# Kernel tuning notes

Measured on AMD Instinct MI355X. Metric: run time of the kernel, lower is better.

Reference implementation:

```python
import jax, jax.numpy as jnp
from jax import lax
import numpy as np

MEM_SZ = 1024
SOMA_FAST = 4.0
SOMA_SLOW = 7.0
MOD_BIAS = 0.4
EPS_BASE = 0.9
BIAS_MOD_RANGE = 5.0


def setup_inputs() -> dict:
    key = jax.random.key(0)
    k1, k2, k3 = jax.random.split(key, 3)
    B, L, IN = 128, 512, 512
    u = jax.random.normal(k1, (B, L, IN), dtype=jnp.float32)
    h0 = jnp.zeros((2, B, MEM_SZ), dtype=jnp.float32)
    W_im = jax.random.normal(k2, (2 * MEM_SZ, IN), dtype=jnp.float32) * 0.05
    b_im = jax.random.normal(k3, (2 * MEM_SZ,), dtype=jnp.float32) * 0.05
    return {"u": u, "h0": h0, "W_im": W_im, "b_im": b_im}


def reference(u, h0, W_im, b_im):
    # Hoisted input projection: one big GEMM over all timesteps.
    # in_emb: [B, L, 2*mem]
    in_emb = jnp.einsum('bli,oi->blo', u, W_im) + b_im
    c1 = in_emb[..., :MEM_SZ]          # soma_bias_contribution_1
    i_o = in_emb[..., MEM_SZ:]
    soma_bias = jnp.tanh(c1 / BIAS_MOD_RANGE) * BIAS_MOD_RANGE

    def step(carry, inp):
        hf, hs = carry
        sb, io = inp
        hfn = jnp.tanh(io + SOMA_FAST * hf
                       - SOMA_SLOW * jnp.square(hs + MOD_BIAS) + sb)
        # variable_eps: 0.9 + 0.9 / (1 + exp((hf - 0.5) / -0.1))
        eps = EPS_BASE + EPS_BASE * jax.nn.sigmoid((hf - 0.5) * 10.0)
        hsn = (1.0 - eps) * hs + eps * hf
        return (hfn, hsn), hfn

    # scan over time: inputs as [L, B, mem]
    xs = (jnp.transpose(soma_bias, (1, 0, 2)), jnp.transpose(i_o, (1, 0, 2)))
    (hf_last, _hs_last), hf_seq = lax.scan(step, (h0[0], h0[1]), xs)
    h_t = jnp.transpose(hf_seq, (1, 0, 2))  # [B, L, mem]
    return h_t, hf_last
```

## Files before the change

kernel.cpp:

```cpp
#include <hip/hip_runtime.h>
#include <hip/hip_fp16.h>

#define MEM  1024
#define B_   128
#define L_   512
#define M_   (B_*L_)
#define N_   (2*MEM)
#define K_   512

#define SCALE_U 16.0f
#define SCALE_W 1024.0f
#define INV_SCALE (1.0f / (16.0f * 1024.0f))

typedef __attribute__((ext_vector_type(8))) _Float16 half8;
typedef __attribute__((ext_vector_type(4))) float f32x4;

__device__ __forceinline__ float fast_tanh(float x) {
    float e = __expf(2.0f * x);
    return 1.0f - 2.0f / (e + 1.0f);
}
__device__ __forceinline__ float fast_sigmoid(float x) {
    return 1.0f / (1.0f + __expf(-x));
}
__device__ __forceinline__ void gl_lds16(const void* g, void* l) {
    __builtin_amdgcn_global_load_lds(
        (const __attribute__((address_space(1))) void*)g,
        (__attribute__((address_space(3))) void*)l, 16, 0, 0);
}

__global__ void split_fp32_fp16x2(const float* __restrict__ in,
                                  unsigned short* __restrict__ hi,
                                  unsigned short* __restrict__ lo,
                                  int n4, float scale) {
    int i = blockIdx.x * 256 + threadIdx.x;
    if (i >= n4) return;
    const float4 v = reinterpret_cast<const float4*>(in)[i];
    float vs[4] = {v.x, v.y, v.z, v.w};
    unsigned short hs_[4], ls_[4];
#pragma unroll
    for (int c = 0; c < 4; ++c) {
        float xs = vs[c] * scale;
        __half h = __float2half_rn(xs);
        float r = xs - __half2float(h);
        __half l = __float2half_rn(r);
        hs_[c] = __half_as_ushort(h);
        ls_[c] = __half_as_ushort(l);
    }
    ushort4 h4, l4;
    h4.x = hs_[0]; h4.y = hs_[1]; h4.z = hs_[2]; h4.w = hs_[3];
    l4.x = ls_[0]; l4.y = ls_[1]; l4.z = ls_[2]; l4.w = ls_[3];
    reinterpret_cast<ushort4*>(hi)[i] = h4;
    reinterpret_cast<ushort4*>(lo)[i] = l4;
}

#define TM 128
#define TN 128
#define BK 32
__global__ __launch_bounds__(256, 2) void gemm_paired_kernel(
    const float* __restrict__ u,
    const unsigned short* __restrict__ wh, const unsigned short* __restrict__ wl,
    const float* __restrict__ bias,
    float* __restrict__ z_out) {
    __shared__ __attribute__((aligned(16))) float Af[TM * BK];
    __shared__ __attribute__((aligned(16))) unsigned short Bh0[TN * BK];
    __shared__ __attribute__((aligned(16))) unsigned short Bl0[TN * BK];
    __shared__ __attribute__((aligned(16))) unsigned short Bh1[TN * BK];
    __shared__ __attribute__((aligned(16))) unsigned short Bl1[TN * BK];

    const int tid = threadIdx.x;
    const int id  = blockIdx.x;
    const int mt  = (id >> 6) * 8 + (id & 7);
    const int nt  = (id >> 3) & 7;
    const int tileM = mt * TM;
    const int tileN = nt * TN;

    const int lane = tid & 63, w = tid >> 6;
    const int wm = w & 1, wn = w >> 1;
    const int lrow = lane & 15, quad = lane >> 4;
    const int q2 = quad ^ ((lrow >> 1) & 3);

    f32x4 acc0[4][4] = {};
    f32x4 acc1[4][4] = {};

    size_t aoff[4];
#pragma unroll
    for (int c = 0; c < 4; ++c) {
        const int p = c * 256 + tid;
        const int row = p >> 3;
        const int chunk = (p & 7) ^ (row & 7);
        aoff[c] = (size_t)(tileM + row) * K_ + chunk * 4;
    }
    const int i0 = tid, i1 = tid + 256;
    const int r0 = i0 >> 2, gs0 = (i0 & 3) ^ ((r0 >> 1) & 3);
    const int r1 = i1 >> 2, gs1 = (i1 & 3) ^ ((r1 >> 1) & 3);
    const size_t sB0a = (size_t)(tileN + r0) * K_ + gs0 * 8;
    const size_t sB0b = (size_t)(tileN + r1) * K_ + gs1 * 8;
    const size_t sB1a = (size_t)(tileN + 1024 + r0) * K_ + gs0 * 8;
    const size_t sB1b = (size_t)(tileN + 1024 + r1) * K_ + gs1 * 8;

    for (int kt = 0; kt < K_ / BK; ++kt) {
        const size_t ko = (size_t)kt * BK;
        __syncthreads();
#pragma unroll
        for (int c = 0; c < 4; ++c)
            gl_lds16(u + aoff[c] + ko, &Af[c * 1024 + tid * 4]);
        gl_lds16(wh + sB0a + ko, &Bh0[i0 * 8]);
        gl_lds16(wh + sB0b + ko, &Bh0[i1 * 8]);
        gl_lds16(wl + sB0a + ko, &Bl0[i0 * 8]);
        gl_lds16(wl + sB0b + ko, &Bl0[i1 * 8]);
        gl_lds16(wh + sB1a + ko, &Bh1[i0 * 8]);
        gl_lds16(wh + sB1b + ko, &Bh1[i1 * 8]);
        gl_lds16(wl + sB1a + ko, &Bl1[i0 * 8]);
        gl_lds16(wl + sB1b + ko, &Bl1[i1 * 8]);
        __syncthreads();

        half8 ahf[4], alf[4];
#pragma unroll
        for (int i = 0; i < 4; ++i) {
            const int r = wm * 64 + i * 16 + lrow;
            const int sw = r & 7;
            const f32x4 t0 = *(const f32x4*)&Af[(r * 8 + ((quad * 2)     ^ sw)) * 4];
            const f32x4 t1 = *(const f32x4*)&Af[(r * 8 + ((quad * 2 + 1) ^ sw)) * 4];
            half8 h, l;
#pragma unroll
            for (int e = 0; e < 4; ++e) {
                float xs = t0[e] * SCALE_U;
                _Float16 hh = (_Float16)xs;
                h[e] = hh;
                l[e] = (_Float16)(xs - (float)hh);
                xs = t1[e] * SCALE_U;
                hh = (_Float16)xs;
                h[e + 4] = hh;
                l[e + 4] = (_Float16)(xs - (float)hh);
            }
            ahf[i] = h; alf[i] = l;
        }
#pragma unroll
        for (int j = 0; j < 4; ++j) {
            const int bo = ((wn * 64 + j * 16 + lrow) * 4 + q2) * 8;
            const half8 b0h = *(const half8*)&Bh0[bo];
            const half8 b0l = *(const half8*)&Bl0[bo];
            const half8 b1h = *(const half8*)&Bh1[bo];
            const half8 b1l = *(const half8*)&Bl1[bo];
#pragma unroll
            for (int i = 0; i < 4; ++i) {
                f32x4 c0 = acc0[i][j];
                c0 = __builtin_amdgcn_mfma_f32_16x16x32_f16(ahf[i], b0h, c0, 0, 0, 0);
                c0 = __builtin_amdgcn_mfma_f32_16x16x32_f16(ahf[i], b0l, c0, 0, 0, 0);
                c0 = __builtin_amdgcn_mfma_f32_16x16x32_f16(alf[i], b0h, c0, 0, 0, 0);
                acc0[i][j] = c0;
                f32x4 c1 = acc1[i][j];
                c1 = __builtin_amdgcn_mfma_f32_16x16x32_f16(ahf[i], b1h, c1, 0, 0, 0);
                c1 = __builtin_amdgcn_mfma_f32_16x16x32_f16(ahf[i], b1l, c1, 0, 0, 0);
                c1 = __builtin_amdgcn_mfma_f32_16x16x32_f16(alf[i], b1h, c1, 0, 0, 0);
                acc1[i][j] = c1;
            }
        }
    }

#pragma unroll
    for (int j = 0; j < 4; ++j) {
        const int c = tileN + wn * 64 + j * 16 + lrow;
        const float b1v = bias[c];
        const float b2v = bias[c + 1024];
#pragma unroll
        for (int i = 0; i < 4; ++i) {
            const int rowb = tileM + wm * 64 + i * 16 + quad * 4;
#pragma unroll
            for (int r = 0; r < 4; ++r) {
                float v1 = acc0[i][j][r] * INV_SCALE + b1v;
                v1 = fast_tanh(v1 * 0.2f) * 5.0f;
                const float v2 = acc1[i][j][r] * INV_SCALE + b2v;
                z_out[(size_t)(rowb + r) * MEM + c] = v1 + v2;
            }
        }
    }
}

__global__ __launch_bounds__(256) void scan_kernel(
    const float* __restrict__ z,
    float* __restrict__ h_t,
    const float* __restrict__ h0,
    float* __restrict__ hf_last) {
    const int idx = blockIdx.x * 256 + threadIdx.x;
    const int b = idx >> 10, m = idx & (MEM - 1);
    float hf = h0[idx];
    float hs = h0[B_ * MEM + idx];
    const size_t base = (size_t)b * L_ * MEM + m;

    float zv[16], zn[16];
#pragma unroll
    for (int j = 0; j < 16; ++j) zv[j] = z[base + (size_t)j * MEM];

    for (int l0 = 0; l0 < L_; l0 += 16) {
        const bool more = (l0 + 16) < L_;
        if (more) {
#pragma unroll
            for (int j = 0; j < 16; ++j)
                zn[j] = z[base + (size_t)(l0 + 16 + j) * MEM];
        }
#pragma unroll
        for (int j = 0; j < 16; ++j) {
            const float hsb = hs + 0.4f;
            const float x = zv[j] + 4.0f * hf - 7.0f * hsb * hsb;
            const float hfn = fast_tanh(x);
            const float eps = 0.9f + 0.9f * fast_sigmoid(10.0f * (hf - 0.5f));
            hs = hs + eps * (hf - hs);
            h_t[base + (size_t)(l0 + j) * MEM] = hfn;
            hf = hfn;
        }
        if (more) {
#pragma unroll
            for (int j = 0; j < 16; ++j) zv[j] = zn[j];
        }
    }
    hf_last[idx] = hf;
}

extern "C" void kernel_launch(void* const* d_in, const int* in_sizes, int n_in,
                              void* d_out, int out_size, void* d_ws, size_t ws_size,
                              hipStream_t stream) {
    const float* u    = (const float*)d_in[0];
    const float* h0   = (const float*)d_in[1];
    const float* W_im = (const float*)d_in[2];
    const float* b_im = (const float*)d_in[3];

    float* out = (float*)d_out;
    float* h_t = out;
    float* hf_last = out + (size_t)M_ * MEM;

    char* ws = (char*)d_ws;
    float* z           = (float*)ws;
    unsigned short* wh = (unsigned short*)(ws + 268435456ull);
    unsigned short* wl = (unsigned short*)(ws + 270532608ull);

    {
        const int n4_w = (N_ * K_) / 4;
        split_fp32_fp16x2<<<(n4_w + 255) / 256, 256, 0, stream>>>(W_im, wh, wl, n4_w, SCALE_W);
    }
    {
        gemm_paired_kernel<<<4096, 256, 0, stream>>>(u, wh, wl, b_im, z);
    }
    {
        scan_kernel<<<(B_ * MEM) / 256, 256, 0, stream>>>(z, h_t, h0, hf_last);
    }
}
```

Before: 770.4 us.

## Double-buffer GEMM LDS tiles and enlarge M tile to 256 with 512 threads

The paired-fp16 GEMM now uses two LDS buffers. Global-to-LDS loads for the next K slice are issued before computing on the current one, which overlaps memory latency with MFMA work and removes one barrier per K step. The M tile doubles to 256 rows with 8 waves per block, halving the grid, and the MFMA section is wrapped in s_setprio to favour matrix issue. LDS per block grows to about 128KB, so only one block fits per CU, which may reduce latency hiding across blocks.

```diff
diff --git a/kernel.cpp b/kernel.cpp
--- a/kernel.cpp
+++ b/kernel.cpp
@@ -53,19 +53,19 @@
     reinterpret_cast<ushort4*>(lo)[i] = l4;
 }
 
-#define TM 128
+#define TM 256
 #define TN 128
 #define BK 32
-__global__ __launch_bounds__(256, 2) void gemm_paired_kernel(
+__global__ __launch_bounds__(512, 2) void gemm_paired_kernel(
     const float* __restrict__ u,
     const unsigned short* __restrict__ wh, const unsigned short* __restrict__ wl,
     const float* __restrict__ bias,
     float* __restrict__ z_out) {
-    __shared__ __attribute__((aligned(16))) float Af[TM * BK];
-    __shared__ __attribute__((aligned(16))) unsigned short Bh0[TN * BK];
-    __shared__ __attribute__((aligned(16))) unsigned short Bl0[TN * BK];
-    __shared__ __attribute__((aligned(16))) unsigned short Bh1[TN * BK];
-    __shared__ __attribute__((aligned(16))) unsigned short Bl1[TN * BK];
+    __shared__ __attribute__((aligned(16))) float Af[2][TM * BK];
+    __shared__ __attribute__((aligned(16))) unsigned short Bh0[2][TN * BK];
+    __shared__ __attribute__((aligned(16))) unsigned short Bl0[2][TN * BK];
+    __shared__ __attribute__((aligned(16))) unsigned short Bh1[2][TN * BK];
+    __shared__ __attribute__((aligned(16))) unsigned short Bl1[2][TN * BK];
 
     const int tid = threadIdx.x;
     const int id  = blockIdx.x;
@@ -75,7 +75,7 @@
     const int tileN = nt * TN;
 
     const int lane = tid & 63, w = tid >> 6;
-    const int wm = w & 1, wn = w >> 1;
+    const int wm = w & 3, wn = w >> 2;
     const int lrow = lane & 15, quad = lane >> 4;
     const int q2 = quad ^ ((lrow >> 1) & 3);
 
@@ -85,77 +85,88 @@
     size_t aoff[4];
 #pragma unroll
     for (int c = 0; c < 4; ++c) {
-        const int p = c * 256 + tid;
+        const int p = c * 512 + tid;
         const int row = p >> 3;
         const int chunk = (p & 7) ^ (row & 7);
         aoff[c] = (size_t)(tileM + row) * K_ + chunk * 4;
     }
-    const int i0 = tid, i1 = tid + 256;
-    const int r0 = i0 >> 2, gs0 = (i0 & 3) ^ ((r0 >> 1) & 3);
-    const int r1 = i1 >> 2, gs1 = (i1 & 3) ^ ((r1 >> 1) & 3);
-    const size_t sB0a = (size_t)(tileN + r0) * K_ + gs0 * 8;
-    const size_t sB0b = (size_t)(tileN + r1) * K_ + gs1 * 8;
-    const size_t sB1a = (size_t)(tileN + 1024 + r0) * K_ + gs0 * 8;
-    const size_t sB1b = (size_t)(tileN + 1024 + r1) * K_ + gs1 * 8;
-
-    for (int kt = 0; kt < K_ / BK; ++kt) {
-        const size_t ko = (size_t)kt * BK;
-        __syncthreads();
-#pragma unroll
-        for (int c = 0; c < 4; ++c)
-            gl_lds16(u + aoff[c] + ko, &Af[c * 1024 + tid * 4]);
-        gl_lds16(wh + sB0a + ko, &Bh0[i0 * 8]);
-        gl_lds16(wh + sB0b + ko, &Bh0[i1 * 8]);
-        gl_lds16(wl + sB0a + ko, &Bl0[i0 * 8]);
-        gl_lds16(wl + sB0b + ko, &Bl0[i1 * 8]);
-        gl_lds16(wh + sB1a + ko, &Bh1[i0 * 8]);
-        gl_lds16(wh + sB1b + ko, &Bh1[i1 * 8]);
-        gl_lds16(wl + sB1a + ko, &Bl1[i0 * 8]);
-        gl_lds16(wl + sB1b + ko, &Bl1[i1 * 8]);
-        __syncthreads();
-
-        half8 ahf[4], alf[4];
-#pragma unroll
-        for (int i = 0; i < 4; ++i) {
-            const int r = wm * 64 + i * 16 + lrow;
-            const int sw = r & 7;
-            const f32x4 t0 = *(const f32x4*)&Af[(r * 8 + ((quad * 2)     ^ sw)) * 4];
-            const f32x4 t1 = *(const f32x4*)&Af[(r * 8 + ((quad * 2 + 1) ^ sw)) * 4];
-            half8 h, l;
-#pragma unroll
-            for (int e = 0; e < 4; ++e) {
-                float xs = t0[e] * SCALE_U;
-                _Float16 hh = (_Float16)xs;
-                h[e] = hh;
-                l[e] = (_Float16)(xs - (float)hh);
-                xs = t1[e] * SCALE_U;
-                hh = (_Float16)xs;
-                h[e + 4] = hh;
-                l[e + 4] = (_Float16)(xs - (float)hh);
-            }
-            ahf[i] = h; alf[i] = l;
-        }
-#pragma unroll
-        for (int j = 0; j < 4; ++j) {
-            const int bo = ((wn * 64 + j * 16 + lrow) * 4 + q2) * 8;
-            const half8 b0h = *(const half8*)&Bh0[bo];
-            const half8 b0l = *(const half8*)&Bl0[bo];
-            const half8 b1h = *(const half8*)&Bh1[bo];
-            const half8 b1l = *(const half8*)&Bl1[bo];
-#pragma unroll
-            for (int i = 0; i < 4; ++i) {
-                f32x4 c0 = acc0[i][j];
-                c0 = __builtin_amdgcn_mfma_f32_16x16x32_f16(ahf[i], b0h, c0, 0, 0, 0);
-                c0 = __builtin_amdgcn_mfma_f32_16x16x32_f16(ahf[i], b0l, c0, 0, 0, 0);
-                c0 = __builtin_amdgcn_mfma_f32_16x16x32_f16(alf[i], b0h, c0, 0, 0, 0);
-                acc0[i][j] = c0;
-                f32x4 c1 = acc1[i][j];
-                c1 = __builtin_amdgcn_mfma_f32_16x16x32_f16(ahf[i], b1h, c1, 0, 0, 0);
-                c1 = __builtin_amdgcn_mfma_f32_16x16x32_f16(ahf[i], b1l, c1, 0, 0, 0);
-                c1 = __builtin_amdgcn_mfma_f32_16x16x32_f16(alf[i], b1h, c1, 0, 0, 0);
-                acc1[i][j] = c1;
-            }
-        }
+    const int rB = tid >> 2;
+    const int gsB = (tid & 3) ^ ((rB >> 1) & 3);
+    const size_t sB0 = (size_t)(tileN + rB) * K_ + gsB * 8;
+    const size_t sB1 = (size_t)(tileN + 1024 + rB) * K_ + gsB * 8;
+
+#define STAGE(BUF, KT) do {                                               \
+        const size_t ko_ = (size_t)(KT) * BK;                             \
+        _Pragma("unroll")                                                 \
+        for (int c = 0; c < 4; ++c)                                       \
+            gl_lds16(u + aoff[c] + ko_, &Af[BUF][(c * 512 + tid) * 4]);   \
+        gl_lds16(wh + sB0 + ko_, &Bh0[BUF][tid * 8]);                     \
+        gl_lds16(wl + sB0 + ko_, &Bl0[BUF][tid * 8]);                     \
+        gl_lds16(wh + sB1 + ko_, &Bh1[BUF][tid * 8]);                     \
+        gl_lds16(wl + sB1 + ko_, &Bl1[BUF][tid * 8]);                     \
+    } while (0)
+
+#define COMPUTE(BUF) do {                                                            \
+        half8 ahf[4], alf[4];                                                        \
+        _Pragma("unroll")                                                            \
+        for (int i = 0; i < 4; ++i) {                                                \
+            const int r = wm * 64 + i * 16 + lrow;                                   \
+            const int sw = r & 7;                                                    \
+            const f32x4 t0 = *(const f32x4*)&Af[BUF][(r * 8 + ((quad * 2)     ^ sw)) * 4]; \
+            const f32x4 t1 = *(const f32x4*)&Af[BUF][(r * 8 + ((quad * 2 + 1) ^ sw)) * 4]; \
+            half8 h, l;                                                              \
+            _Pragma("unroll")                                                        \
+            for (int e = 0; e < 4; ++e) {                                            \
+                float xs = t0[e] * SCALE_U;                                          \
+                _Float16 hh = (_Float16)xs;                                          \
+                h[e] = hh;                                                           \
+                l[e] = (_Float16)(xs - (float)hh);                                   \
+                xs = t1[e] * SCALE_U;                                                \
+                hh = (_Float16)xs;                                                   \
+                h[e + 4] = hh;                                                       \
+                l[e + 4] = (_Float16)(xs - (float)hh);                               \
+            }                                                                        \
+            ahf[i] = h; alf[i] = l;                                                  \
+        }                                                                            \
+        __builtin_amdgcn_s_setprio(1);                                               \
+        _Pragma("unroll")                                                            \
+        for (int j = 0; j < 4; ++j) {                                                \
+            const int bo = ((wn * 64 + j * 16 + lrow) * 4 + q2) * 8;                 \
+            const half8 b0h = *(const half8*)&Bh0[BUF][bo];                          \
+            const half8 b0l = *(const half8*)&Bl0[BUF][bo];                          \
+            const half8 b1h = *(const half8*)&Bh1[BUF][bo];                          \
+            const half8 b1l = *(const half8*)&Bl1[BUF][bo];                          \
+            _Pragma("unroll")                                                        \
+            for (int i = 0; i < 4; ++i) {                                            \
+                f32x4 c0 = acc0[i][j];                                               \
+                c0 = __builtin_amdgcn_mfma_f32_16x16x32_f16(ahf[i], b0h, c0, 0, 0, 0); \
+                c0 = __builtin_amdgcn_mfma_f32_16x16x32_f16(ahf[i], b0l, c0, 0, 0, 0); \
+                c0 = __builtin_amdgcn_mfma_f32_16x16x32_f16(alf[i], b0h, c0, 0, 0, 0); \
+                acc0[i][j] = c0;                                                     \
+                f32x4 c1 = acc1[i][j];                                               \
+                c1 = __builtin_amdgcn_mfma_f32_16x16x32_f16(ahf[i], b1h, c1, 0, 0, 0); \
+                c1 = __builtin_amdgcn_mfma_f32_16x16x32_f16(ahf[i], b1l, c1, 0, 0, 0); \
+                c1 = __builtin_amdgcn_mfma_f32_16x16x32_f16(alf[i], b1h, c1, 0, 0, 0); \
+                acc1[i][j] = c1;                                                     \
+            }                                                                        \
+        }                                                                            \
+        __builtin_amdgcn_s_setprio(0);                                               \
+    } while (0)
+
+    STAGE(0, 0);
+    asm volatile("s_waitcnt vmcnt(0)" ::: "memory");
+    __builtin_amdgcn_s_barrier();
+
+#pragma unroll 1
+    for (int kt = 0; kt < K_ / BK; kt += 2) {
+        STAGE(1, kt + 1);
+        COMPUTE(0);
+        asm volatile("s_waitcnt vmcnt(0)" ::: "memory");
+        __builtin_amdgcn_s_barrier();
+        if (kt + 2 < K_ / BK) STAGE(0, kt + 2);
+        COMPUTE(1);
+        asm volatile("s_waitcnt vmcnt(0)" ::: "memory");
+        __builtin_amdgcn_s_barrier();
     }
 
 #pragma unroll
@@ -175,6 +186,8 @@
             }
         }
     }
+#undef STAGE
+#undef COMPUTE
 }
 
 __global__ __launch_bounds__(256) void scan_kernel(
@@ -239,7 +252,7 @@
         split_fp32_fp16x2<<<(n4_w + 255) / 256, 256, 0, stream>>>(W_im, wh, wl, n4_w, SCALE_W);
     }
     {
-        gemm_paired_kernel<<<4096, 256, 0, stream>>>(u, wh, wl, b_im, z);
+        gemm_paired_kernel<<<2048, 512, 0, stream>>>(u, wh, wl, b_im, z);
     }
     {
         scan_kernel<<<(B_ * MEM) / 256, 256, 0, stream>>>(z, h_t, h0, hf_last);
```

Result: slower. 842.5 us (+9.4%).
